# Optimization experiments

Hardware: AMD Instinct MI355X
Metric: run time of the kernel (lower is better)

## Reference

```python
import jax, jax.numpy as jnp
import numpy as np

B, S, HID, NH = 2, 2048, 1024, 16
HD = HID // NH  # 64


def setup_inputs() -> dict:
    key = jax.random.key(0)
    ks = jax.random.split(key, 10)
    sc = 0.02
    return {
        "hidden_states": jax.random.normal(ks[0], (B, S, HID), jnp.float32),
        "attention_mask": jnp.zeros((B, 1, 1, S), jnp.float32),
        "struct_attn_mask": jax.random.normal(ks[1], (B, S, S), jnp.float32),
        "Wq": jax.random.normal(ks[2], (HID, HID), jnp.float32) * sc,
        "bq": jnp.zeros((HID,), jnp.float32),
        "Wk": jax.random.normal(ks[3], (HID, HID), jnp.float32) * sc,
        "bk": jnp.zeros((HID,), jnp.float32),
        "Wv": jax.random.normal(ks[4], (HID, HID), jnp.float32) * sc,
        "bv": jnp.zeros((HID,), jnp.float32),
        "struct_gate": jnp.full((NH,), 0.1, jnp.float32),
    }


def _heads(x):
    # [B,S,HID] -> [B,NH,S,HD]
    return x.reshape(B, S, NH, HD).transpose(0, 2, 1, 3)


def reference(hidden_states, attention_mask, struct_attn_mask, Wq, bq, Wk, bk, Wv, bv, struct_gate):
    q = _heads(hidden_states @ Wq.T + bq)
    k = _heads(hidden_states @ Wk.T + bk)
    v = _heads(hidden_states @ Wv.T + bv)
    scores = jnp.einsum("bhqd,bhkd->bhqk", q, k) / np.sqrt(HD).astype(np.float32)
    scores = scores + attention_mask
    scores = scores + struct_attn_mask[:, None, :, :] * struct_gate[None, :, None, None]
    probs = jax.nn.softmax(scores, axis=-1)  # dropout p=0 (eval) -> no-op
    ctx = jnp.einsum("bhqk,bhkd->bhqd", probs, v)
    ctx = ctx.transpose(0, 2, 1, 3).reshape(B, S, HID)
    return (ctx,)
```

## Files before the change

kernel.cpp:

```cpp
#include <hip/hip_runtime.h>
#include <hip/hip_bf16.h>
#include <cmath>

#define S_LEN 2048
#define HIDN  1024
#define NHEAD 16
#define HDIM  64
#define NBAT  2

static constexpr long NA = (long)NBAT * S_LEN * HIDN;
static constexpr long NW = (long)HIDN * HIDN;
static constexpr long NM = (long)NBAT * S_LEN * S_LEN;
static constexpr long NAM = (long)NBAT * S_LEN;

typedef __attribute__((ext_vector_type(8))) __bf16 bf16x8;
typedef __attribute__((ext_vector_type(4))) float f32x4;
typedef __attribute__((ext_vector_type(16))) float f32x16;
typedef __attribute__((ext_vector_type(4))) unsigned short u16x4;

#define LOG2E 1.44269504088896340736f

__device__ __forceinline__ unsigned short f2bf(float f) {
  __hip_bfloat16 h = __float2bfloat16(f);
  unsigned short u;
  __builtin_memcpy(&u, &h, 2);
  return u;
}

__device__ __forceinline__ float bfu2f(unsigned short u) {
  unsigned v = (unsigned)u << 16;
  float f;
  __builtin_memcpy(&f, &v, 4);
  return f;
}

__device__ __forceinline__ unsigned cvtpk(float a, float b) {
  unsigned r;
  asm volatile("v_cvt_pk_bf16_f32 %0, %1, %2" : "=v"(r) : "v"(a), "v"(b));
  return r;
}

__device__ __forceinline__ void gload_lds16(const void* g, void* l) {
  __builtin_amdgcn_global_load_lds(
      (const __attribute__((address_space(1))) void*)g,
      (__attribute__((address_space(3))) void*)l, 16, 0, 0);
}

__global__ __launch_bounds__(256) void convert_kernel(
    const float* __restrict__ hs, const float* __restrict__ wq,
    const float* __restrict__ wk, const float* __restrict__ wv,
    const float* __restrict__ mask, const float* __restrict__ amask,
    __hip_bfloat16* __restrict__ Abf, __hip_bfloat16* __restrict__ Wcat,
    __hip_bfloat16* __restrict__ Mbf, float* __restrict__ amg) {
  const long tot4 = (NA + 3 * NW + NM + NAM) >> 2;
  for (long i4 = (long)blockIdx.x * blockDim.x + threadIdx.x; i4 < tot4;
       i4 += (long)gridDim.x * blockDim.x) {
    long i = i4 << 2;
    if (i < NA + 3 * NW + NM) {
      const float* s;
      __hip_bfloat16* dq;
      if (i < NA)               { s = hs + i;                   dq = Abf + i; }
      else if (i < NA + NW)     { s = wq + (i - NA);            dq = Wcat + (i - NA); }
      else if (i < NA + 2 * NW) { s = wk + (i - NA - NW);       dq = Wcat + (i - NA); }
      else if (i < NA + 3 * NW) { s = wv + (i - NA - 2 * NW);   dq = Wcat + (i - NA); }
      else                      { s = mask + (i - NA - 3 * NW); dq = Mbf + (i - NA - 3 * NW); }
      float4 v = *(const float4*)s;
      union { unsigned short u[4]; uint2 p; } o;
      o.u[0] = f2bf(v.x); o.u[1] = f2bf(v.y); o.u[2] = f2bf(v.z); o.u[3] = f2bf(v.w);
      *(uint2*)dq = o.p;
    } else {
      long j = i - (NA + 3 * NW + NM);
      float4 v = *(const float4*)(amask + j);
      v.x *= LOG2E; v.y *= LOG2E; v.z *= LOG2E; v.w *= LOG2E;
      *(float4*)(amg + j) = v;
    }
  }
}

__global__ __launch_bounds__(256) void qkv_gemm(
    const __hip_bfloat16* __restrict__ A, const __hip_bfloat16* __restrict__ Bw,
    const float* __restrict__ bq, const float* __restrict__ bk,
    const float* __restrict__ bv, __hip_bfloat16* __restrict__ qb,
    __hip_bfloat16* __restrict__ kb, __hip_bfloat16* __restrict__ vtb) {
  __shared__ __hip_bfloat16 sA[128 * 32];
  __shared__ __hip_bfloat16 sB[128 * 32];

  int bid = blockIdx.x;
  int cpx = gridDim.x >> 3;
  int wg = (bid & 7) * cpx + (bid >> 3);
  int bm = wg / 24, bn = wg % 24;
  int tid = threadIdx.x, lane = tid & 63, wid = tid >> 6;
  int wr = wid >> 1, wc = wid & 1;
  int lr = lane & 15, hi = lane >> 4;
  int srow = lane >> 2, scol = (lane & 3) * 8;

  f32x4 acc[4][4] = {};

  for (int kt = 0; kt < 32; ++kt) {
    int k0 = kt * 32;
#pragma unroll
    for (int cc = 0; cc < 2; ++cc) {
      int c = wid * 2 + cc;
      const __hip_bfloat16* ga =
          A + ((size_t)(bm * 128 + c * 16 + srow) * 1024 + k0 + scol);
      gload_lds16(ga, (char*)sA + c * 1024);
      const __hip_bfloat16* gb =
          Bw + ((size_t)(bn * 128 + c * 16 + srow) * 1024 + k0 + scol);
      gload_lds16(gb, (char*)sB + c * 1024);
    }
    __syncthreads();
    bf16x8 af[4], bf[4];
#pragma unroll
    for (int mt = 0; mt < 4; ++mt)
      af[mt] = *(const bf16x8*)((const char*)sA +
                                ((wr * 64 + mt * 16 + lr) * 32 + hi * 8) * 2);
#pragma unroll
    for (int nt = 0; nt < 4; ++nt)
      bf[nt] = *(const bf16x8*)((const char*)sB +
                                ((wc * 64 + nt * 16 + lr) * 32 + hi * 8) * 2);
#pragma unroll
    for (int mt = 0; mt < 4; ++mt)
#pragma unroll
      for (int nt = 0; nt < 4; ++nt)
        acc[mt][nt] =
            __builtin_amdgcn_mfma_f32_16x16x32_bf16(af[mt], bf[nt], acc[mt][nt], 0, 0, 0);
    __syncthreads();
  }

  const float c2 = LOG2E / 8.0f;
#pragma unroll
  for (int nt = 0; nt < 4; ++nt) {
    int nb = bn * 128 + wc * 64 + nt * 16;
    int t = nb >> 10;
    int rem = nb & 1023;
    const float* bp = (t == 0) ? bq : (t == 1) ? bk : bv;
    float scl = (t == 0) ? c2 : 1.0f;
    int h = rem >> 6, d0r = rem & 63;
    float bias = bp[rem + lr];
    int d = d0r + lr;
#pragma unroll
    for (int mt = 0; mt < 4; ++mt) {
      int m0 = bm * 128 + wr * 64 + mt * 16 + hi * 4;
      int b = m0 >> 11, s = m0 & 2047;
      if (t == 2) {
        union { unsigned short u[4]; uint2 p; } o;
#pragma unroll
        for (int r = 0; r < 4; ++r) o.u[r] = f2bf(acc[mt][nt][r] + bias);
        *(uint2*)(vtb + (((size_t)(b * NHEAD + h) * HDIM + d) * S_LEN + s)) = o.p;
      } else {
        __hip_bfloat16* ob = (t == 0) ? qb : kb;
#pragma unroll
        for (int r = 0; r < 4; ++r) {
          size_t off = (((size_t)(b * NHEAD + h)) * S_LEN + (s + r)) * HDIM + d;
          ob[off] = __float2bfloat16((acc[mt][nt][r] + bias) * scl);
        }
      }
    }
  }
}

__global__ __launch_bounds__(512, 4) void attn_kernel(
    const __hip_bfloat16* __restrict__ qb, const __hip_bfloat16* __restrict__ kbuf,
    const __hip_bfloat16* __restrict__ vt, const __hip_bfloat16* __restrict__ Mbf,
    const float* __restrict__ amg, const float* __restrict__ gate,
    float* __restrict__ out) {
  __shared__ alignas(16) char smem[73728];
  __shared__ float mlb[4][2][32];

  int bid = blockIdx.x;
  int wg = (bid & 7) * 64 + (bid >> 3);
  int bi = wg >> 8;
  int h = (wg >> 4) & 15;
  int qt = wg & 15;
  int bh = bi * NHEAD + h;

  int tid = threadIdx.x;
  int lane = tid & 63, wid = tid >> 6;
  int grp = wid >> 2, w4 = wid & 3;
  int l31 = lane & 31, hi2 = lane >> 5;
  int qbase = qt * 128 + w4 * 32;
  int qrow = qbase + l31;
  int kbase = grp << 10;
  float g2 = gate[h] * LOG2E;

  const char* Kb = (const char*)kbuf + (size_t)bh * S_LEN * 128;
  const char* Vb = (const char*)vt + (size_t)bh * HDIM * S_LEN * 2;
  const char* Mrow = (const char*)Mbf + ((size_t)bi * S_LEN + qrow) * S_LEN * 2 + hi2 * 8;

  bf16x8 qf[4];
  {
    const __hip_bfloat16* qp = qb + ((size_t)bh * S_LEN + qrow) * HDIM + hi2 * 8;
#pragma unroll
    for (int dc = 0; dc < 4; ++dc) qf[dc] = *(const bf16x8*)(qp + dc * 16);
  }

  int r8 = lane >> 3, ch = lane & 7;
  float* amL = (float*)(smem + 65536 + grp * 4096);

  auto stage = [&](int buf, int t) {
    int k0 = kbase + t * 64;
    char* kdst = smem + buf * 32768 + grp * 16384 + w4 * 2048;
    char* vdst = kdst + 8192;
#pragma unroll
    for (int c = 0; c < 2; ++c) {
      int row = w4 * 16 + c * 8 + r8;
      gload_lds16(Kb + (size_t)(k0 + row) * 128 + ((ch ^ r8) << 4), kdst + c * 1024);
      gload_lds16(Vb + (size_t)row * 4096 + (size_t)k0 * 2 + ((ch ^ r8) << 4),
                  vdst + c * 1024);
    }
  };

  u16x4 mn0[4], mn1[4];
#pragma unroll
  for (int rp = 0; rp < 4; ++rp) {
    mn0[rp] = *(const u16x4*)(Mrow + (size_t)(kbase + rp * 8) * 2);
    mn1[rp] = *(const u16x4*)(Mrow + (size_t)(kbase + 32 + rp * 8) * 2);
  }

  stage(0, 0);
  gload_lds16((const char*)amg + ((size_t)bi * S_LEN + kbase + w4 * 256) * 4,
              (char*)amL + w4 * 1024);
  __syncthreads();

  f32x16 O = {}, O2 = {};
  float m = -INFINITY, l = 0.f;

  for (int t = 0; t < 16; ++t) {
    int cur = t & 1;
    if (t < 15) stage(cur ^ 1, t + 1);
    const char* sK = smem + cur * 32768 + grp * 16384;
    const char* sV = sK + 8192;

#pragma unroll
    for (int ss = 0; ss < 2; ++ss) {
      int klocal = t * 64 + ss * 32;

      f32x16 st;
#pragma unroll
      for (int rp = 0; rp < 4; ++rp) {
        float4 am = *(const float4*)(amL + klocal + rp * 8 + hi2 * 4);
        union { u16x4 v; unsigned short e[4]; } mv;
        mv.v = ss ? mn1[rp] : mn0[rp];
        st[rp * 4 + 0] = fmaf(bfu2f(mv.e[0]), g2, am.x);
        st[rp * 4 + 1] = fmaf(bfu2f(mv.e[1]), g2, am.y);
        st[rp * 4 + 2] = fmaf(bfu2f(mv.e[2]), g2, am.z);
        st[rp * 4 + 3] = fmaf(bfu2f(mv.e[3]), g2, am.w);
      }

      if (t < 15) {
        int kn = kbase + (t + 1) * 64 + ss * 32;
#pragma unroll
        for (int rp = 0; rp < 4; ++rp) {
          u16x4 nv = *(const u16x4*)(Mrow + (size_t)(kn + rp * 8) * 2);
          if (ss) mn1[rp] = nv; else mn0[rp] = nv;
        }
      }

#pragma unroll
      for (int dc = 0; dc < 4; ++dc) {
        int row = ss * 32 + l31;
        bf16x8 kf = *(const bf16x8*)(sK + row * 128 +
                                     (((dc * 2 + hi2) ^ (l31 & 7)) << 4));
        st = __builtin_amdgcn_mfma_f32_32x32x16_bf16(kf, qf[dc], st, 0, 0, 0);
      }

      float pmax = -3.4e38f;
#pragma unroll
      for (int rp = 0; rp < 4; ++rp)
        pmax = fmaxf(pmax, fmaxf(fmaxf(st[rp * 4 + 0], st[rp * 4 + 1]),
                                 fmaxf(st[rp * 4 + 2], st[rp * 4 + 3])));
      pmax = fmaxf(pmax, __shfl_xor(pmax, 32));
      if (__any(pmax > m + 8.f)) {
        float mnew = fmaxf(m, pmax);
        float alpha = exp2f(m - mnew);
        m = mnew;
        l *= alpha;
        O *= alpha;
        O2 *= alpha;
      }

      float rs0 = 0.f, rs1 = 0.f, rs2 = 0.f, rs3 = 0.f;
#pragma unroll
      for (int rp = 0; rp < 4; ++rp) {
        float p0 = exp2f(st[rp * 4 + 0] - m);
        float p1 = exp2f(st[rp * 4 + 1] - m);
        float p2 = exp2f(st[rp * 4 + 2] - m);
        float p3 = exp2f(st[rp * 4 + 3] - m);
        st[rp * 4 + 0] = p0; st[rp * 4 + 1] = p1;
        st[rp * 4 + 2] = p2; st[rp * 4 + 3] = p3;
        rs0 += p0; rs1 += p1; rs2 += p2; rs3 += p3;
      }
      float rs = (rs0 + rs1) + (rs2 + rs3);
      rs += __shfl_xor(rs, 32);
      l += rs;

#pragma unroll
      for (int ks = 0; ks < 2; ++ks) {
        int rp = ks * 2;
        unsigned A0 = cvtpk(st[rp * 4 + 0], st[rp * 4 + 1]);
        unsigned A1 = cvtpk(st[rp * 4 + 2], st[rp * 4 + 3]);
        unsigned B0 = cvtpk(st[rp * 4 + 4], st[rp * 4 + 5]);
        unsigned B1 = cvtpk(st[rp * 4 + 6], st[rp * 4 + 7]);
        asm volatile("v_permlane32_swap_b32 %0, %1" : "+v"(A0), "+v"(B0));
        asm volatile("v_permlane32_swap_b32 %0, %1" : "+v"(A1), "+v"(B1));
        union { unsigned w[4]; bf16x8 v; } Bf;
        Bf.w[0] = A0; Bf.w[1] = A1; Bf.w[2] = B0; Bf.w[3] = B1;
        int vc = ss * 4 + ks * 2 + hi2;
        bf16x8 v0 = *(const bf16x8*)(sV + l31 * 128 + ((vc ^ (l31 & 7)) << 4));
        bf16x8 v1 = *(const bf16x8*)(sV + (32 + l31) * 128 + ((vc ^ (l31 & 7)) << 4));
        O = __builtin_amdgcn_mfma_f32_32x32x16_bf16(v0, Bf.v, O, 0, 0, 0);
        O2 = __builtin_amdgcn_mfma_f32_32x32x16_bf16(v1, Bf.v, O2, 0, 0, 0);
      }
    }
    __syncthreads();
  }

  float* mbuf = (float*)smem + w4 * (32 * 68);
  if (grp == 1) {
    if (hi2 == 0) { mlb[w4][0][l31] = m; mlb[w4][1][l31] = l; }
#pragma unroll
    for (int dt = 0; dt < 2; ++dt)
#pragma unroll
      for (int rq = 0; rq < 4; ++rq) {
        int d0 = dt * 32 + 8 * rq + 4 * hi2;
        const f32x16& Ox = dt ? O2 : O;
        f32x4 v = {Ox[rq * 4 + 0], Ox[rq * 4 + 1], Ox[rq * 4 + 2], Ox[rq * 4 + 3]};
        *(f32x4*)(mbuf + l31 * 68 + d0) = v;
      }
  }
  __syncthreads();
  if (grp == 0) {
    float m1 = mlb[w4][0][l31], l1 = mlb[w4][1][l31];
    float mx = fmaxf(m, m1);
    float a0 = exp2f(m - mx), a1 = exp2f(m1 - mx);
    float linv = 1.0f / (a0 * l + a1 * l1);
    a0 *= linv; a1 *= linv;
    float* orow = out + ((size_t)bi * S_LEN + qrow) * HIDN + h * HDIM;
#pragma unroll
    for (int dt = 0; dt < 2; ++dt)
#pragma unroll
      for (int rq = 0; rq < 4; ++rq) {
        int d0 = dt * 32 + 8 * rq + 4 * hi2;
        const f32x16& Ox = dt ? O2 : O;
        f32x4 v1 = *(const f32x4*)(mbuf + l31 * 68 + d0);
        float4 o;
        o.x = Ox[rq * 4 + 0] * a0 + v1[0] * a1;
        o.y = Ox[rq * 4 + 1] * a0 + v1[1] * a1;
        o.z = Ox[rq * 4 + 2] * a0 + v1[2] * a1;
        o.w = Ox[rq * 4 + 3] * a0 + v1[3] * a1;
        *(float4*)(orow + d0) = o;
      }
  }
}

extern "C" void kernel_launch(void* const* d_in, const int* in_sizes, int n_in,
                              void* d_out, int out_size, void* d_ws, size_t ws_size,
                              hipStream_t stream) {
  const float* hs    = (const float*)d_in[0];
  const float* amask = (const float*)d_in[1];
  const float* smask = (const float*)d_in[2];
  const float* Wq    = (const float*)d_in[3];
  const float* bq    = (const float*)d_in[4];
  const float* Wk    = (const float*)d_in[5];
  const float* bk    = (const float*)d_in[6];
  const float* Wv    = (const float*)d_in[7];
  const float* bv    = (const float*)d_in[8];
  const float* gate  = (const float*)d_in[9];

  char* ws = (char*)d_ws;
  __hip_bfloat16* Abf  = (__hip_bfloat16*)(ws);
  __hip_bfloat16* Wcat = (__hip_bfloat16*)(ws + 8388608);
  __hip_bfloat16* qb   = (__hip_bfloat16*)(ws + 8388608 + 6291456);
  __hip_bfloat16* kb   = qb + NA;
  __hip_bfloat16* vtr  = kb + NA;
  __hip_bfloat16* Mbf  = vtr + NA;
  float*          amg  = (float*)(Mbf + NM);

  convert_kernel<<<2048, 256, 0, stream>>>(hs, Wq, Wk, Wv, smask, amask, Abf, Wcat, Mbf, amg);
  qkv_gemm<<<768, 256, 0, stream>>>(Abf, Wcat, bq, bk, bv, qb, kb, vtr);
  attn_kernel<<<512, 512, 0, stream>>>(qb, kb, vtr, Mbf, amg, gate, (float*)d_out);
}
```

Before: 137.2 us.

## Process full 64-key tile per softmax step with interleaved QK MFMAs and max3

Restructures the inner attention loop so both 32-key halves of each 64-key tile are scored together: the two independent QK^T MFMA chains are interleaved, and one online-softmax rescale/max/sum step covers 64 keys instead of two. The row max uses v_max3_f32, and s_setprio raises wave priority around the MFMA sections. This halves the rescale checks and cross-lane shuffles and exposes more MFMA parallelism. The cost is more live registers (two 16-float score tiles), which could reduce occupancy or cause spills.

```diff
diff --git a/kernel.cpp b/kernel.cpp
--- a/kernel.cpp
+++ b/kernel.cpp
@@ -37,6 +37,12 @@
 __device__ __forceinline__ unsigned cvtpk(float a, float b) {
   unsigned r;
   asm volatile("v_cvt_pk_bf16_f32 %0, %1, %2" : "=v"(r) : "v"(a), "v"(b));
+  return r;
+}
+
+__device__ __forceinline__ float max3f(float a, float b, float c) {
+  float r;
+  asm("v_max3_f32 %0, %1, %2, %3" : "=v"(r) : "v"(a), "v"(b), "v"(c));
   return r;
 }
 
@@ -230,77 +236,105 @@
     if (t < 15) stage(cur ^ 1, t + 1);
     const char* sK = smem + cur * 32768 + grp * 16384;
     const char* sV = sK + 8192;
-
+    int klocal = t * 64;
+
+    f32x16 st0, st1;
+#pragma unroll
+    for (int rp = 0; rp < 4; ++rp) {
+      float4 am0 = *(const float4*)(amL + klocal + rp * 8 + hi2 * 4);
+      float4 am1 = *(const float4*)(amL + klocal + 32 + rp * 8 + hi2 * 4);
+      union { u16x4 v; unsigned short e[4]; } mv0, mv1;
+      mv0.v = mn0[rp]; mv1.v = mn1[rp];
+      st0[rp * 4 + 0] = fmaf(bfu2f(mv0.e[0]), g2, am0.x);
+      st0[rp * 4 + 1] = fmaf(bfu2f(mv0.e[1]), g2, am0.y);
+      st0[rp * 4 + 2] = fmaf(bfu2f(mv0.e[2]), g2, am0.z);
+      st0[rp * 4 + 3] = fmaf(bfu2f(mv0.e[3]), g2, am0.w);
+      st1[rp * 4 + 0] = fmaf(bfu2f(mv1.e[0]), g2, am1.x);
+      st1[rp * 4 + 1] = fmaf(bfu2f(mv1.e[1]), g2, am1.y);
+      st1[rp * 4 + 2] = fmaf(bfu2f(mv1.e[2]), g2, am1.z);
+      st1[rp * 4 + 3] = fmaf(bfu2f(mv1.e[3]), g2, am1.w);
+    }
+
+    if (t < 15) {
+      int kn = kbase + (t + 1) * 64;
+#pragma unroll
+      for (int rp = 0; rp < 4; ++rp) {
+        mn0[rp] = *(const u16x4*)(Mrow + (size_t)(kn + rp * 8) * 2);
+        mn1[rp] = *(const u16x4*)(Mrow + (size_t)(kn + 32 + rp * 8) * 2);
+      }
+    }
+
+    __builtin_amdgcn_s_setprio(1);
+#pragma unroll
+    for (int dc = 0; dc < 4; ++dc) {
+      bf16x8 kf0 = *(const bf16x8*)(sK + l31 * 128 +
+                                    (((dc * 2 + hi2) ^ (l31 & 7)) << 4));
+      st0 = __builtin_amdgcn_mfma_f32_32x32x16_bf16(kf0, qf[dc], st0, 0, 0, 0);
+      bf16x8 kf1 = *(const bf16x8*)(sK + (32 + l31) * 128 +
+                                    (((dc * 2 + hi2) ^ (l31 & 7)) << 4));
+      st1 = __builtin_amdgcn_mfma_f32_32x32x16_bf16(kf1, qf[dc], st1, 0, 0, 0);
+    }
+    __builtin_amdgcn_s_setprio(0);
+
+    float x0 = max3f(st0[0], st0[1], st0[2]);
+    float x1 = max3f(st0[3], st0[4], st0[5]);
+    float x2 = max3f(st0[6], st0[7], st0[8]);
+    float x3 = max3f(st0[9], st0[10], st0[11]);
+    float x4 = max3f(st0[12], st0[13], st0[14]);
+    float x5 = max3f(st0[15], st1[0], st1[1]);
+    float x6 = max3f(st1[2], st1[3], st1[4]);
+    float x7 = max3f(st1[5], st1[6], st1[7]);
+    float x8 = max3f(st1[8], st1[9], st1[10]);
+    float x9 = max3f(st1[11], st1[12], st1[13]);
+    float y0 = max3f(st1[14], st1[15], x0);
+    float y1 = max3f(x1, x2, x3);
+    float y2 = max3f(x4, x5, x6);
+    float y3 = max3f(x7, x8, x9);
+    float pmax = fmaxf(max3f(y0, y1, y2), y3);
+    pmax = fmaxf(pmax, __shfl_xor(pmax, 32));
+    if (__any(pmax > m + 8.f)) {
+      float mnew = fmaxf(m, pmax);
+      float alpha = exp2f(m - mnew);
+      m = mnew;
+      l *= alpha;
+      O *= alpha;
+      O2 *= alpha;
+    }
+
+    float rs0 = 0.f, rs1 = 0.f, rs2 = 0.f, rs3 = 0.f;
+    float rs4 = 0.f, rs5 = 0.f, rs6 = 0.f, rs7 = 0.f;
+#pragma unroll
+    for (int rp = 0; rp < 4; ++rp) {
+      float p0 = exp2f(st0[rp * 4 + 0] - m);
+      float p1 = exp2f(st0[rp * 4 + 1] - m);
+      float p2 = exp2f(st0[rp * 4 + 2] - m);
+      float p3 = exp2f(st0[rp * 4 + 3] - m);
+      st0[rp * 4 + 0] = p0; st0[rp * 4 + 1] = p1;
+      st0[rp * 4 + 2] = p2; st0[rp * 4 + 3] = p3;
+      rs0 += p0; rs1 += p1; rs2 += p2; rs3 += p3;
+      float q0 = exp2f(st1[rp * 4 + 0] - m);
+      float q1 = exp2f(st1[rp * 4 + 1] - m);
+      float q2 = exp2f(st1[rp * 4 + 2] - m);
+      float q3 = exp2f(st1[rp * 4 + 3] - m);
+      st1[rp * 4 + 0] = q0; st1[rp * 4 + 1] = q1;
+      st1[rp * 4 + 2] = q2; st1[rp * 4 + 3] = q3;
+      rs4 += q0; rs5 += q1; rs6 += q2; rs7 += q3;
+    }
+    float rs = ((rs0 + rs1) + (rs2 + rs3)) + ((rs4 + rs5) + (rs6 + rs7));
+    rs += __shfl_xor(rs, 32);
+    l += rs;
+
+    __builtin_amdgcn_s_setprio(1);
 #pragma unroll
     for (int ss = 0; ss < 2; ++ss) {
-      int klocal = t * 64 + ss * 32;
-
-      f32x16 st;
-#pragma unroll
-      for (int rp = 0; rp < 4; ++rp) {
-        float4 am = *(const float4*)(amL + klocal + rp * 8 + hi2 * 4);
-        union { u16x4 v; unsigned short e[4]; } mv;
-        mv.v = ss ? mn1[rp] : mn0[rp];
-        st[rp * 4 + 0] = fmaf(bfu2f(mv.e[0]), g2, am.x);
-        st[rp * 4 + 1] = fmaf(bfu2f(mv.e[1]), g2, am.y);
-        st[rp * 4 + 2] = fmaf(bfu2f(mv.e[2]), g2, am.z);
-        st[rp * 4 + 3] = fmaf(bfu2f(mv.e[3]), g2, am.w);
-      }
-
-      if (t < 15) {
-        int kn = kbase + (t + 1) * 64 + ss * 32;
-#pragma unroll
-        for (int rp = 0; rp < 4; ++rp) {
-          u16x4 nv = *(const u16x4*)(Mrow + (size_t)(kn + rp * 8) * 2);
-          if (ss) mn1[rp] = nv; else mn0[rp] = nv;
-        }
-      }
-
-#pragma unroll
-      for (int dc = 0; dc < 4; ++dc) {
-        int row = ss * 32 + l31;
-        bf16x8 kf = *(const bf16x8*)(sK + row * 128 +
-                                     (((dc * 2 + hi2) ^ (l31 & 7)) << 4));
-        st = __builtin_amdgcn_mfma_f32_32x32x16_bf16(kf, qf[dc], st, 0, 0, 0);
-      }
-
-      float pmax = -3.4e38f;
-#pragma unroll
-      for (int rp = 0; rp < 4; ++rp)
-        pmax = fmaxf(pmax, fmaxf(fmaxf(st[rp * 4 + 0], st[rp * 4 + 1]),
-                                 fmaxf(st[rp * 4 + 2], st[rp * 4 + 3])));
-      pmax = fmaxf(pmax, __shfl_xor(pmax, 32));
-      if (__any(pmax > m + 8.f)) {
-        float mnew = fmaxf(m, pmax);
-        float alpha = exp2f(m - mnew);
-        m = mnew;
-        l *= alpha;
-        O *= alpha;
-        O2 *= alpha;
-      }
-
-      float rs0 = 0.f, rs1 = 0.f, rs2 = 0.f, rs3 = 0.f;
-#pragma unroll
-      for (int rp = 0; rp < 4; ++rp) {
-        float p0 = exp2f(st[rp * 4 + 0] - m);
-        float p1 = exp2f(st[rp * 4 + 1] - m);
-        float p2 = exp2f(st[rp * 4 + 2] - m);
-        float p3 = exp2f(st[rp * 4 + 3] - m);
-        st[rp * 4 + 0] = p0; st[rp * 4 + 1] = p1;
-        st[rp * 4 + 2] = p2; st[rp * 4 + 3] = p3;
-        rs0 += p0; rs1 += p1; rs2 += p2; rs3 += p3;
-      }
-      float rs = (rs0 + rs1) + (rs2 + rs3);
-      rs += __shfl_xor(rs, 32);
-      l += rs;
-
+      const f32x16& sts = ss ? st1 : st0;
 #pragma unroll
       for (int ks = 0; ks < 2; ++ks) {
         int rp = ks * 2;
-        unsigned A0 = cvtpk(st[rp * 4 + 0], st[rp * 4 + 1]);
-        unsigned A1 = cvtpk(st[rp * 4 + 2], st[rp * 4 + 3]);
-        unsigned B0 = cvtpk(st[rp * 4 + 4], st[rp * 4 + 5]);
-        unsigned B1 = cvtpk(st[rp * 4 + 6], st[rp * 4 + 7]);
+        unsigned A0 = cvtpk(sts[rp * 4 + 0], sts[rp * 4 + 1]);
+        unsigned A1 = cvtpk(sts[rp * 4 + 2], sts[rp * 4 + 3]);
+        unsigned B0 = cvtpk(sts[rp * 4 + 4], sts[rp * 4 + 5]);
+        unsigned B1 = cvtpk(sts[rp * 4 + 6], sts[rp * 4 + 7]);
         asm volatile("v_permlane32_swap_b32 %0, %1" : "+v"(A0), "+v"(B0));
         asm volatile("v_permlane32_swap_b32 %0, %1" : "+v"(A1), "+v"(B1));
         union { unsigned w[4]; bf16x8 v; } Bf;
@@ -312,6 +346,7 @@
         O2 = __builtin_amdgcn_mfma_f32_32x32x16_bf16(v1, Bf.v, O2, 0, 0, 0);
       }
     }
+    __builtin_amdgcn_s_setprio(0);
     __syncthreads();
   }
 
```

Result: slower. 174.0 us (+26.9%).
